# Performance work log

Measured on AMD Instinct MI355X. Metric: run time of the kernel, lower is better.

## Reference

```python
import jax, jax.numpy as jnp
import numpy as np

NR, NQ, NH, NV = 256, 64, 64, 4
B = 8192
NDRAW = 12
# zoneout probabilities from __init__ (applied deterministically, eval-mode expectation)
ZO_IJ, ZO_ID, ZO_GJ, ZO_GD = 0.3, 0.2, 0.3, 0.2


def _lin_init(key, fan_in, fan_out):
    kw, kb = jax.random.split(key)
    s = 1.0 / np.sqrt(fan_in)
    W = jax.random.uniform(kw, (fan_in, fan_out), jnp.float32, -s, s)
    b = jax.random.uniform(kb, (fan_out,), jnp.float32, -s, s)
    return W, b


def setup_inputs() -> dict:
    key = jax.random.key(0)
    ks = jax.random.split(key, 16)
    inp = {"ndraw": NDRAW}
    inp["cnd_repr"] = jax.random.normal(ks[0], (B, NR), jnp.float32)
    inp["qry_jrep"] = jax.random.normal(ks[1], (B, NQ), jnp.float32)
    inp["qry_drep"] = jax.random.normal(ks[2], (B, NQ), jnp.float32)
    inp["qry_v"] = jax.random.normal(ks[3], (B, NV), jnp.float32)
    for n in ["hi_j", "ci_j", "oi_j", "hi_d", "ci_d", "oi_d",
              "hg_j", "cg_j", "og_j", "hg_d", "cg_d", "og_d", "ug_j", "ug_d"]:
        inp[n] = jnp.zeros((B, NH), jnp.float32)
    # LSTM cells: W [in+nh, 4*nh]
    inp["W_ij"], inp["b_ij"] = _lin_init(ks[4], NR + NQ + NH + NH, 4 * NH)
    inp["W_id"], inp["b_id"] = _lin_init(ks[5], NR + NQ + NH + NH, 4 * NH)
    inp["W_gj"], inp["b_gj"] = _lin_init(ks[6], NR + NH + NH, 4 * NH)
    inp["W_gd"], inp["b_gd"] = _lin_init(ks[7], NR + NH + NV + NH, 4 * NH)
    # GaussianFactor heads: nh -> (mean, logv)
    inp["W_poj"], inp["b_poj"] = _lin_init(ks[8], NH, 2 * NH)
    inp["W_pod"], inp["b_pod"] = _lin_init(ks[9], NH, 2 * NH)
    inp["W_prj"], inp["b_prj"] = _lin_init(ks[10], NH, 2 * NH)
    inp["W_prd"], inp["b_prd"] = _lin_init(ks[11], NH, 2 * NH)
    # GeneratorDelta: cat(u, h) -> delta
    inp["W_dj"], inp["b_dj"] = _lin_init(ks[12], 2 * NH, NH)
    inp["W_dd"], inp["b_dd"] = _lin_init(ks[13], 2 * NH, NH)
    return inp


def _lstm(x, h, c, W, b, zo):
    g = jnp.concatenate([x, h], axis=1) @ W + b  # [B, 4*NH]
    i, f, gg, o = jnp.split(g, 4, axis=1)
    i, f, o = jax.nn.sigmoid(i), jax.nn.sigmoid(f), jax.nn.sigmoid(o)
    c_new = f * c + i * jnp.tanh(gg)
    h_new = o * jnp.tanh(c_new)
    # deterministic zoneout (expectation form)
    return zo * h + (1.0 - zo) * h_new, zo * c + (1.0 - zo) * c_new, o


def _gauss_stats(h, W, b):
    s = h @ W + b
    mean, logv = jnp.split(s, 2, axis=1)
    return mean, logv


def _delta(u, h, W, b):
    return jax.nn.leaky_relu(jnp.concatenate([u, h], axis=1) @ W + b)


def _forward(ndraw, cnd_repr, qry_jrep, qry_drep, qry_v,
             hi_j, ci_j, oi_j, hi_d, ci_d, oi_d,
             hg_j, cg_j, og_j, hg_d, cg_d, og_d, ug_j, ug_d,
             W_ij, b_ij, W_id, b_id, W_gj, b_gj, W_gd, b_gd,
             W_poj, b_poj, W_pod, b_pod, W_prj, b_prj, W_prd, b_prd,
             W_dj, b_dj, W_dd, b_dd):
    Bn = cnd_repr.shape[0]
    eps_j = jax.random.normal(jax.random.key(1), (ndraw, Bn, NH), jnp.float32)
    eps_d = jax.random.normal(jax.random.key(2), (ndraw, Bn, NH), jnp.float32)

    def step(carry, eps):
        (hi_j, ci_j, oi_j, hi_d, ci_d, oi_d,
         hg_j, cg_j, og_j, hg_d, cg_d, og_d, ug_j, ug_d) = carry
        ej, ed = eps
        # priors from current generator states (sampled z unused in loop)
        pr_m_j, pr_v_j = _gauss_stats(hg_j, W_prj, b_prj)
        pr_m_d, pr_v_d = _gauss_stats(hg_d, W_prd, b_prd)
        # inference states
        inp_ij = jnp.concatenate([cnd_repr, qry_jrep, hg_j], axis=1)
        inp_id = jnp.concatenate([cnd_repr, qry_drep, hg_d], axis=1)
        hi_j, ci_j, oi_j = _lstm(inp_ij, hi_j, ci_j, W_ij, b_ij, ZO_IJ)
        hi_d, ci_d, oi_d = _lstm(inp_id, hi_d, ci_d, W_id, b_id, ZO_ID)
        # posteriors + reparameterized samples
        po_m_j, po_v_j = _gauss_stats(hi_j, W_poj, b_poj)
        po_m_d, po_v_d = _gauss_stats(hi_d, W_pod, b_pod)
        z_j = po_m_j + jnp.exp(0.5 * po_v_j) * ej
        z_d = po_m_d + jnp.exp(0.5 * po_v_d) * ed
        # generator states
        inp_gj = jnp.concatenate([cnd_repr, z_j], axis=1)
        inp_gd = jnp.concatenate([cnd_repr, z_d, qry_v], axis=1)
        hg_j, cg_j, og_j = _lstm(inp_gj, hg_j, cg_j, W_gj, b_gj, ZO_GJ)
        hg_d, cg_d, og_d = _lstm(inp_gd, hg_d, cg_d, W_gd, b_gd, ZO_GD)
        # additive canvas updates
        ug_j = ug_j + _delta(ug_j, hg_j, W_dj, b_dj)
        ug_d = ug_d + _delta(ug_d, hg_d, W_dd, b_dd)
        carry = (hi_j, ci_j, oi_j, hi_d, ci_d, oi_d,
                 hg_j, cg_j, og_j, hg_d, cg_d, og_d, ug_j, ug_d)
        ys = (pr_m_j, pr_v_j, pr_m_d, pr_v_d, po_m_j, po_v_j, po_m_d, po_v_d)
        return carry, ys

    carry0 = (hi_j, ci_j, oi_j, hi_d, ci_d, oi_d,
              hg_j, cg_j, og_j, hg_d, cg_d, og_d, ug_j, ug_d)
    carry, ys = jax.lax.scan(step, carry0, (eps_j, eps_d))
    ug_j_out, ug_d_out = carry[-2], carry[-1]
    # pack: [2 + 8*ndraw, B, NH] (canvases then per-draw prior/posterior stats)
    out = jnp.concatenate([ug_j_out[None], ug_d_out[None]] + list(ys), axis=0)
    return out


def reference(ndraw, cnd_repr, qry_jrep, qry_drep, qry_v,
              hi_j, ci_j, oi_j, hi_d, ci_d, oi_d,
              hg_j, cg_j, og_j, hg_d, cg_d, og_d, ug_j, ug_d,
              W_ij, b_ij, W_id, b_id, W_gj, b_gj, W_gd, b_gd,
              W_poj, b_poj, W_pod, b_pod, W_prj, b_prj, W_prd, b_prd,
              W_dj, b_dj, W_dd, b_dd):
    return _forward(ndraw, cnd_repr, qry_jrep, qry_drep, qry_v,
                    hi_j, ci_j, oi_j, hi_d, ci_d, oi_d,
                    hg_j, cg_j, og_j, hg_d, cg_d, og_d, ug_j, ug_d,
                    W_ij, b_ij, W_id, b_id, W_gj, b_gj, W_gd, b_gd,
                    W_poj, b_poj, W_pod, b_pod, W_prj, b_prj, W_prd, b_prd,
                    W_dj, b_dj, W_dd, b_dd)
```

## Files before the change

kernel.cpp:

```cpp
#include <hip/hip_runtime.h>
#include <hip/hip_bf16.h>


typedef __attribute__((ext_vector_type(8))) short bf16x8;
typedef __attribute__((ext_vector_type(4))) float f32x4;

#define MFMA(A, Bv, C) __builtin_amdgcn_mfma_f32_16x16x32_bf16(A, Bv, C, 0, 0, 0)

#define FR_WI   0
#define FR_WG   32768
#define FR_WPR  65536
#define FR_WPO  73728
#define FR_WD   81920
#define FR_SIDE 90112

__device__ __forceinline__ unsigned short f2bf(float f) {
  unsigned u = __float_as_uint(f);
  return (unsigned short)((u + 0x7FFFu + ((u >> 16) & 1u)) >> 16);
}
__device__ __forceinline__ unsigned pk2(float a, float b) {
  return (unsigned)f2bf(a) | ((unsigned)f2bf(b) << 16);
}
__device__ __forceinline__ float sigf(float x) {
  return 1.0f / (1.0f + __expf(-x));
}
__device__ __forceinline__ float tanh_f(float x) {
  return 1.0f - 2.0f / (__expf(2.0f * x) + 1.0f);
}

__device__ __forceinline__ float eps_threefry(unsigned seed, unsigned idx) {
  unsigned x0 = 0u, x1 = idx;
  const unsigned ks0 = 0u, ks1 = seed, ks2 = seed ^ 0x1BD11BDAu;
  x0 += ks0; x1 += ks1;
#define TF_R(r) { x0 += x1; x1 = (x1 << (r)) | (x1 >> (32 - (r))); x1 ^= x0; }
  TF_R(13) TF_R(15) TF_R(26) TF_R(6)  x0 += ks1; x1 += ks2 + 1u;
  TF_R(17) TF_R(29) TF_R(16) TF_R(24) x0 += ks2; x1 += ks0 + 2u;
  TF_R(13) TF_R(15) TF_R(26) TF_R(6)  x0 += ks0; x1 += ks1 + 3u;
  TF_R(17) TF_R(29) TF_R(16) TF_R(24) x0 += ks1; x1 += ks2 + 4u;
  TF_R(13) TF_R(15) TF_R(26) TF_R(6)  x0 += ks2; x1 += ks0 + 5u;
#undef TF_R
  unsigned bits = x0 ^ x1;
  unsigned fb = (bits >> 9) | 0x3F800000u;
  const float lo = -0.99999994f;
  float f = __uint_as_float(fb) - 1.0f;
  float u = fmaxf(lo, f * 2.0f + lo);
  float w = -log1pf(-u * u);
  float p;
  if (w < 5.0f) {
    w -= 2.5f;
    p = 2.81022636e-08f;
    p = fmaf(p, w, 3.43273939e-07f);
    p = fmaf(p, w, -3.5233877e-06f);
    p = fmaf(p, w, -4.39150654e-06f);
    p = fmaf(p, w, 0.00021858087f);
    p = fmaf(p, w, -0.00125372503f);
    p = fmaf(p, w, -0.00417768164f);
    p = fmaf(p, w, 0.246640727f);
    p = fmaf(p, w, 1.50140941f);
  } else {
    w = sqrtf(w) - 3.0f;
    p = -0.000200214257f;
    p = fmaf(p, w, 0.000100950558f);
    p = fmaf(p, w, 0.00134934322f);
    p = fmaf(p, w, -0.00367342844f);
    p = fmaf(p, w, 0.00573950773f);
    p = fmaf(p, w, -0.0076224613f);
    p = fmaf(p, w, 0.00943887047f);
    p = fmaf(p, w, 1.00167406f);
    p = fmaf(p, w, 2.83297682f);
  }
  return 1.41421356f * (p * u);
}

__global__ __launch_bounds__(256) void GeRN_prepEps(
    const float* __restrict__ Wij, const float* __restrict__ Wid,
    const float* __restrict__ Wgj, const float* __restrict__ Wgd,
    const float* __restrict__ Wprj, const float* __restrict__ Wprd,
    const float* __restrict__ Wpoj, const float* __restrict__ Wpod,
    const float* __restrict__ Wdj, const float* __restrict__ Wdd,
    unsigned short* __restrict__ frB, unsigned short* __restrict__ sBs,
    float* __restrict__ ebuf, unsigned ndBN)
{
  if (blockIdx.x < 236) {
    const int vb = blockIdx.x * 4 + (threadIdx.x >> 6);
    const int l = threadIdx.x & 63;
    if (vb < 352) {
      const int s = vb / 176;
      int tt = vb % 176;
      const float* W; int ldw, rb, NT, kt, nt; size_t doff;
      if (tt < 64)       { W = s ? Wid : Wij; ldw = 256; NT = 16; kt = tt >> 4; nt = tt & 15;
                           rb = 320 + kt * 32; doff = FR_WI; }
      else if (tt < 128) { tt -= 64; W = s ? Wgd : Wgj; ldw = 256; NT = 16; kt = tt >> 4; nt = tt & 15;
                           rb = (kt < 2) ? 256 + kt * 32 : (s ? 324 : 320) + (kt - 2) * 32; doff = FR_WG; }
      else if (tt < 144) { tt -= 128; W = s ? Wprd : Wprj; ldw = 128; NT = 8; kt = tt >> 3; nt = tt & 7;
                           rb = kt * 32; doff = FR_WPR; }
      else if (tt < 160) { tt -= 144; W = s ? Wpod : Wpoj; ldw = 128; NT = 8; kt = tt >> 3; nt = tt & 7;
                           rb = kt * 32; doff = FR_WPO; }
      else               { tt -= 160; W = s ? Wdd : Wdj; ldw = 64; NT = 4; kt = tt >> 2; nt = tt & 3;
                           rb = (kt < 2) ? kt * 32 : 64 + (kt - 2) * 32; doff = FR_WD; }
      unsigned short* dst = frB + (size_t)s * FR_SIDE + doff
                          + ((size_t)(kt * NT + nt) * 64 + l) * 8;
      const int kk = (l >> 4) * 8;
      const int c = nt * 16 + (l & 15);
      #pragma unroll
      for (int j = 0; j < 8; ++j)
        dst[j] = f2bf(W[(size_t)(rb + kk + j) * ldw + c]);
    } else {
      int bb = vb - 352;
      int mat, base;
      if (bb < 160)      { mat = 0; base = 0; }
      else if (bb < 320) { mat = 1; base = 160; }
      else if (bb < 448) { mat = 2; base = 320; }
      else               { mat = 3; base = 448; }
      int tt = bb - base;
      int kk = tt >> 4, nt = tt & 15;
      const float* W = mat == 0 ? Wij : mat == 1 ? Wid : mat == 2 ? Wgj : Wgd;
      const int c = nt * 16 + (l & 15);
      const int kl0 = (l >> 4) * 8;
      unsigned short* dst = sBs + ((size_t)bb * 64 + l) * 8;
      if (mat == 3 && kk == 8) {
        #pragma unroll
        for (int j = 0; j < 8; ++j) {
          int klo = kl0 + j;
          dst[j] = (klo < 4) ? f2bf(W[(size_t)(320 + klo) * 256 + c]) : (unsigned short)0;
        }
      } else {
        int rb = (kk < 8) ? kk * 32 : 256 + (kk - 8) * 32;
        #pragma unroll
        for (int j = 0; j < 8; ++j)
          dst[j] = f2bf(W[(size_t)(rb + kl0 + j) * 256 + c]);
      }
    }
  } else {
    unsigned j0 = ((blockIdx.x - 236) * 256u + threadIdx.x) * 8u;
    const unsigned total = 2u * ndBN;
    if (j0 >= total) return;
    const unsigned s = (j0 >= ndBN) ? 1u : 0u;
    const unsigned i0 = j0 - s * ndBN;
    const unsigned seed = 1u + s;
    float v[8];
    #pragma unroll
    for (int k = 0; k < 8; ++k) v[k] = eps_threefry(seed, i0 + (unsigned)k);
    float4 a = {v[0], v[1], v[2], v[3]};
    float4 b = {v[4], v[5], v[6], v[7]};
    *(float4*)(ebuf + j0) = a;
    *(float4*)(ebuf + j0 + 4) = b;
  }
}

#define WR_FR(buf, row, c, v) \
  fr[buf][(c) >> 5][((row) & 15) + (((c) >> 3) & 3) * 16][(c) & 7] = f2bf(v)
#define LD_FR(buf, kt) (*(const bf16x8*)&fr[buf][kt][l][0])
#define LD_B(off, kt, nt, NT) \
  (*(const bf16x8*)(FB + (off) + (((kt) * (NT) + (nt)) * 64 + l) * 8))
#define LD_S(idx) (*(const bf16x8*)&sBs[((size_t)(idx) * 64 + l) * 8])
#define LD_H(ph, kt, nt) \
  (*(const bf16x8*)&shH[(ph) * 8192 + (((kt) * 8 + (nt)) * 64 + l) * 8])

template<int USE_EPS>
__global__ __launch_bounds__(256, 2) void GeRN_recur(
    const unsigned short* __restrict__ frB,
    const unsigned short* __restrict__ sBs,
    const float* __restrict__ cnd, const float* __restrict__ qjg,
    const float* __restrict__ qdg, const float* __restrict__ qvg,
    const float* __restrict__ bij, const float* __restrict__ bid,
    const float* __restrict__ bgj, const float* __restrict__ bgd,
    const float* __restrict__ bprj, const float* __restrict__ bprd,
    const float* __restrict__ bpoj, const float* __restrict__ bpod,
    const float* __restrict__ bdj,  const float* __restrict__ bdd,
    const float* __restrict__ hi_j0, const float* __restrict__ ci_j0,
    const float* __restrict__ hi_d0, const float* __restrict__ ci_d0,
    const float* __restrict__ hg_j0, const float* __restrict__ cg_j0,
    const float* __restrict__ hg_d0, const float* __restrict__ cg_d0,
    const float* __restrict__ ug_j0, const float* __restrict__ ug_d0,
    const float* __restrict__ eps_buf, unsigned ndBN,
    float* __restrict__ out, int B, int nd)
{
  alignas(16) __shared__ unsigned short fr[6][2][64][8];
  alignas(16) __shared__ unsigned short shH[16384];
  alignas(16) __shared__ unsigned short As[11][64][8];

  const int tid = threadIdx.x;
  const int l   = tid & 63;
  const int wv  = tid >> 6;
  const int s   = blockIdx.x & 1;
  const int rbk = blockIdx.x >> 1;
  const int r0  = (l >> 4) * 4;
  const int col = wv * 16 + (l & 15);
  const int bbase = rbk * 16;
  const size_t BN = (size_t)B * 64;

  const float* hi0 = s ? hi_d0 : hi_j0;  const float* ci0 = s ? ci_d0 : ci_j0;
  const float* hg0 = s ? hg_d0 : hg_j0;  const float* cg0 = s ? cg_d0 : cg_j0;
  const float* ug0 = s ? ug_d0 : ug_j0;
  const float* BPR = s ? bprd : bprj;
  const float* BPO = s ? bpod : bpoj;
  const float* BD  = s ? bdd  : bdj;
  const float* BI  = s ? bid  : bij;
  const float* BG  = s ? bgd  : bgj;
  const float* qq  = s ? qdg  : qjg;
  const unsigned short* FB = frB + (size_t)s * FR_SIDE;

  bf16x8 wi[4][4], wg[4][4], wd[4];
  #pragma unroll
  for (int kt = 0; kt < 4; ++kt) {
    #pragma unroll
    for (int g = 0; g < 4; ++g) {
      wi[kt][g] = LD_B(FR_WI, kt, g * 4 + wv, 16);
      wg[kt][g] = LD_B(FR_WG, kt, g * 4 + wv, 16);
    }
    wd[kt] = LD_B(FR_WD, kt, wv, 4);
  }
  #pragma unroll
  for (int kt = 0; kt < 4; ++kt) {
    #pragma unroll
    for (int g = 0; g < 4; ++g)
      asm volatile("" : "+v"(wi[kt][g]), "+v"(wg[kt][g]));
    asm volatile("" : "+v"(wd[kt]));
  }

  {
    const float4* src = (const float4*)(FB + FR_WPR);
    float4* dst = (float4*)shH;
    for (int i = tid; i < 2048; i += 256) dst[i] = src[i];
  }
  for (int i = tid; i < 16 * 44; i += 256) {
    int r = i / 44, kc = i % 44;
    float v[8];
    if (kc < 32) {
      const float4* p = (const float4*)&cnd[(size_t)(bbase + r) * 256 + kc * 8];
      float4 x0 = p[0], x1 = p[1];
      v[0] = x0.x; v[1] = x0.y; v[2] = x0.z; v[3] = x0.w;
      v[4] = x1.x; v[5] = x1.y; v[6] = x1.z; v[7] = x1.w;
    } else if (kc < 40) {
      const float4* p = (const float4*)&qq[(size_t)(bbase + r) * 64 + (kc - 32) * 8];
      float4 x0 = p[0], x1 = p[1];
      v[0] = x0.x; v[1] = x0.y; v[2] = x0.z; v[3] = x0.w;
      v[4] = x1.x; v[5] = x1.y; v[6] = x1.z; v[7] = x1.w;
    } else if (kc == 40 && s) {
      #pragma unroll
      for (int j = 0; j < 8; ++j) v[j] = (j < 4) ? qvg[(size_t)(bbase + r) * 4 + j] : 0.0f;
    } else {
      #pragma unroll
      for (int j = 0; j < 8; ++j) v[j] = 0.0f;
    }
    int kt = kc >> 2;
    int lane = r + (kc & 3) * 16;
    uint4 wq;
    wq.x = pk2(v[0], v[1]); wq.y = pk2(v[2], v[3]);
    wq.z = pk2(v[4], v[5]); wq.w = pk2(v[6], v[7]);
    *(uint4*)&As[kt][lane][0] = wq;
  }
  __syncthreads();

  f32x4 preI[4], preG[4];
  {
    const int ktB_I = s ? 160 : 0;
    const int ktB_G = s ? 448 : 320;
    const int ktN_G = s ? 9 : 8;
    #pragma unroll
    for (int g = 0; g < 4; ++g) {
      float bi = BI[g * 64 + col];
      float bg = BG[g * 64 + col];
      f32x4 vi = {bi, bi, bi, bi};
      f32x4 vg = {bg, bg, bg, bg};
      preI[g] = vi; preG[g] = vg;
    }
    #pragma unroll
    for (int kk = 0; kk < 10; ++kk) {
      bf16x8 a = *(const bf16x8*)&As[kk][l][0];
      #pragma unroll
      for (int g = 0; g < 4; ++g)
        preI[g] = MFMA(a, LD_S(ktB_I + kk * 16 + g * 4 + wv), preI[g]);
    }
    for (int kk = 0; kk < ktN_G; ++kk) {
      int ktA = (kk < 8) ? kk : 10;
      bf16x8 a = *(const bf16x8*)&As[ktA][l][0];
      #pragma unroll
      for (int g = 0; g < 4; ++g)
        preG[g] = MFMA(a, LD_S(ktB_G + kk * 16 + g * 4 + wv), preG[g]);
    }
  }

  float hi_[4], ci_[4], hg_[4], cg_[4], u_[4];
  #pragma unroll
  for (int r = 0; r < 4; ++r) {
    size_t gi = (size_t)(bbase + r0 + r) * 64 + col;
    hi_[r] = hi0[gi]; ci_[r] = ci0[gi];
    hg_[r] = hg0[gi]; cg_[r] = cg0[gi];
    u_[r]  = ug0[gi];
  }
  const float bprm = BPR[col], bprv = BPR[64 + col];
  const float bpom = BPO[col], bpov = BPO[64 + col];
  const float bd   = BD[col];

  #pragma unroll
  for (int r = 0; r < 4; ++r) {
    WR_FR(0, r0 + r, col, hi_[r]);
    WR_FR(2, r0 + r, col, hg_[r]);
    WR_FR(4, r0 + r, col, u_[r]);
  }
  __syncthreads();

  const float zo = s ? 0.2f : 0.3f, zo1 = 1.0f - zo;

  const unsigned gi0 = (unsigned)((bbase + r0) * 64 + col);
  float* o_prm = out + (size_t)(2 + (2 * s) * nd) * BN + gi0;
  float* o_prv = out + (size_t)(2 + (2 * s + 1) * nd) * BN + gi0;
  float* o_pom = out + (size_t)(2 + (4 + 2 * s) * nd) * BN + gi0;
  float* o_pov = out + (size_t)(2 + (5 + 2 * s) * nd) * BN + gi0;
  unsigned e0 = gi0;
  const unsigned BNu = (unsigned)BN;
  const unsigned eseed = 1u + (unsigned)s;
  const float* ep = USE_EPS ? (eps_buf + (size_t)s * ndBN + gi0) : (const float*)0;

  for (int t = 0; t < nd; ++t) {
    const int cb = t & 1;
    float epre[4];
    if (USE_EPS) {
      #pragma unroll
      for (int r = 0; r < 4; ++r) epre[r] = ep[r * 64];
    }
    bf16x8 a_hg0 = LD_FR(2, 0), a_hg1 = LD_FR(2, 1);
    bf16x8 a_hi0 = LD_FR(cb, 0), a_hi1 = LD_FR(cb, 1);

    {
      f32x4 am = {bprm, bprm, bprm, bprm};
      f32x4 av = {bprv, bprv, bprv, bprv};
      am = MFMA(a_hg0, LD_H(0, 0, wv), am);
      am = MFMA(a_hg1, LD_H(0, 1, wv), am);
      av = MFMA(a_hg0, LD_H(0, 0, wv + 4), av);
      av = MFMA(a_hg1, LD_H(0, 1, wv + 4), av);
      #pragma unroll
      for (int r = 0; r < 4; ++r) {
        o_prm[r * 64] = am[r];
        o_prv[r * 64] = av[r];
      }
    }
    {
      f32x4 acc[4];
      #pragma unroll
      for (int g = 0; g < 4; ++g) acc[g] = preI[g];
      #pragma unroll
      for (int g = 0; g < 4; ++g) {
        acc[g] = MFMA(a_hg0, wi[0][g], acc[g]);
        acc[g] = MFMA(a_hg1, wi[1][g], acc[g]);
        acc[g] = MFMA(a_hi0, wi[2][g], acc[g]);
        acc[g] = MFMA(a_hi1, wi[3][g], acc[g]);
      }
      #pragma unroll
      for (int r = 0; r < 4; ++r) {
        float ig = sigf(acc[0][r]), fg = sigf(acc[1][r]);
        float gg = tanh_f(acc[2][r]), og = sigf(acc[3][r]);
        float cn = fmaf(fg, ci_[r], ig * gg);
        float hn = og * tanh_f(cn);
        hi_[r] = fmaf(zo, hi_[r], zo1 * hn);
        ci_[r] = fmaf(zo, ci_[r], zo1 * cn);
        WR_FR(cb ^ 1, r0 + r, col, hi_[r]);
      }
    }
    __syncthreads();

    {
      bf16x8 a0 = LD_FR(cb ^ 1, 0), a1 = LD_FR(cb ^ 1, 1);
      f32x4 am = {bpom, bpom, bpom, bpom};
      f32x4 av = {bpov, bpov, bpov, bpov};
      am = MFMA(a0, LD_H(1, 0, wv), am);
      am = MFMA(a1, LD_H(1, 1, wv), am);
      av = MFMA(a0, LD_H(1, 0, wv + 4), av);
      av = MFMA(a1, LD_H(1, 1, wv + 4), av);
      #pragma unroll
      for (int r = 0; r < 4; ++r) {
        o_pom[r * 64] = am[r];
        o_pov[r * 64] = av[r];
        float e = USE_EPS ? epre[r] : eps_threefry(eseed, e0 + r * 64);
        float z = fmaf(__expf(0.5f * av[r]), e, am[r]);
        WR_FR(3, r0 + r, col, z);
      }
    }
    __syncthreads();

    {
      bf16x8 az0 = LD_FR(3, 0), az1 = LD_FR(3, 1);
      f32x4 acc[4];
      #pragma unroll
      for (int g = 0; g < 4; ++g) acc[g] = preG[g];
      #pragma unroll
      for (int g = 0; g < 4; ++g) {
        acc[g] = MFMA(az0,   wg[0][g], acc[g]);
        acc[g] = MFMA(az1,   wg[1][g], acc[g]);
        acc[g] = MFMA(a_hg0, wg[2][g], acc[g]);
        acc[g] = MFMA(a_hg1, wg[3][g], acc[g]);
      }
      #pragma unroll
      for (int r = 0; r < 4; ++r) {
        float ig = sigf(acc[0][r]), fg = sigf(acc[1][r]);
        float gg = tanh_f(acc[2][r]), og = sigf(acc[3][r]);
        float cn = fmaf(fg, cg_[r], ig * gg);
        float hn = og * tanh_f(cn);
        hg_[r] = fmaf(zo, hg_[r], zo1 * hn);
        cg_[r] = fmaf(zo, cg_[r], zo1 * cn);
        WR_FR(2, r0 + r, col, hg_[r]);
      }
    }
    __syncthreads();

    {
      bf16x8 au0 = LD_FR(4 + cb, 0), au1 = LD_FR(4 + cb, 1);
      bf16x8 ah0 = LD_FR(2, 0), ah1 = LD_FR(2, 1);
      f32x4 acc = {bd, bd, bd, bd};
      acc = MFMA(au0, wd[0], acc);
      acc = MFMA(au1, wd[1], acc);
      acc = MFMA(ah0, wd[2], acc);
      acc = MFMA(ah1, wd[3], acc);
      #pragma unroll
      for (int r = 0; r < 4; ++r) {
        float a = acc[r];
        float d = a > 0.0f ? a : 0.01f * a;
        u_[r] += d;
        WR_FR(4 + (cb ^ 1), r0 + r, col, u_[r]);
      }
    }
    __syncthreads();

    o_prm += BN; o_prv += BN; o_pom += BN; o_pov += BN;
    e0 += BNu;
    if (USE_EPS) ep += BN;
  }

  #pragma unroll
  for (int r = 0; r < 4; ++r) {
    size_t gi = (size_t)(bbase + r0 + r) * 64 + col;
    out[(size_t)s * BN + gi] = u_[r];
  }
}

extern "C" void kernel_launch(void* const* d_in, const int* in_sizes, int n_in,
                              void* d_out, int out_size, void* d_ws, size_t ws_size,
                              hipStream_t stream)
{
  const float* cnd = (const float*)d_in[1];
  const float* qj  = (const float*)d_in[2];
  const float* qd  = (const float*)d_in[3];
  const float* qv  = (const float*)d_in[4];
  const float* hi_j0 = (const float*)d_in[5];
  const float* ci_j0 = (const float*)d_in[6];
  const float* hi_d0 = (const float*)d_in[8];
  const float* ci_d0 = (const float*)d_in[9];
  const float* hg_j0 = (const float*)d_in[11];
  const float* cg_j0 = (const float*)d_in[12];
  const float* hg_d0 = (const float*)d_in[14];
  const float* cg_d0 = (const float*)d_in[15];
  const float* ug_j0 = (const float*)d_in[17];
  const float* ug_d0 = (const float*)d_in[18];
  const float* Wij = (const float*)d_in[19]; const float* bij = (const float*)d_in[20];
  const float* Wid = (const float*)d_in[21]; const float* bid = (const float*)d_in[22];
  const float* Wgj = (const float*)d_in[23]; const float* bgj = (const float*)d_in[24];
  const float* Wgd = (const float*)d_in[25]; const float* bgd = (const float*)d_in[26];
  const float* Wpoj = (const float*)d_in[27]; const float* bpoj = (const float*)d_in[28];
  const float* Wpod = (const float*)d_in[29]; const float* bpod = (const float*)d_in[30];
  const float* Wprj = (const float*)d_in[31]; const float* bprj = (const float*)d_in[32];
  const float* Wprd = (const float*)d_in[33]; const float* bprd = (const float*)d_in[34];
  const float* Wdj = (const float*)d_in[35]; const float* bdj = (const float*)d_in[36];
  const float* Wdd = (const float*)d_in[37]; const float* bdd = (const float*)d_in[38];

  const int B = in_sizes[1] / 256;
  const int slots = out_size / (B * 64);
  const int nd = (slots - 2) / 8;

  unsigned short* frB = (unsigned short*)d_ws;
  unsigned short* sBs = frB + 2 * FR_SIDE;
  size_t epsOff = (size_t)2 * FR_SIDE * 2 + (size_t)592 * 512 * 2;
  epsOff = (epsOff + 255) & ~(size_t)255;
  const unsigned ndBN = (unsigned)((size_t)nd * B * 64);
  float* epsBuf = (float*)((char*)d_ws + epsOff);
  const bool useEps = ws_size >= epsOff + (size_t)2 * ndBN * 4;
  float* out = (float*)d_out;

  const int epsBlocks = useEps ? (int)((2u * ndBN + 2047u) / 2048u) : 0;
  GeRN_prepEps<<<236 + epsBlocks, 256, 0, stream>>>(
      Wij, Wid, Wgj, Wgd, Wprj, Wprd, Wpoj, Wpod, Wdj, Wdd, frB, sBs,
      epsBuf, ndBN);
  if (useEps) {
    GeRN_recur<1><<<2 * (B / 16), 256, 0, stream>>>(
        frB, sBs, cnd, qj, qd, qv, bij, bid, bgj, bgd,
        bprj, bprd, bpoj, bpod, bdj, bdd,
        hi_j0, ci_j0, hi_d0, ci_d0, hg_j0, cg_j0, hg_d0, cg_d0, ug_j0, ug_d0,
        epsBuf, ndBN, out, B, nd);
  } else {
    GeRN_recur<0><<<2 * (B / 16), 256, 0, stream>>>(
        frB, sBs, cnd, qj, qd, qv, bij, bid, bgj, bgd,
        bprj, bprd, bpoj, bpod, bdj, bdd,
        hi_j0, ci_j0, hi_d0, ci_d0, hg_j0, cg_j0, hg_d0, cg_d0, ug_j0, ug_d0,
        (const float*)0, ndBN, out, B, nd);
  }
}
```

Baseline: 204.6 us.

## Stream recurrent weights from global memory instead of registers and LDS

After: 478.1 us. 2.34x slower.

```diff
diff --git a/kernel.cpp b/kernel.cpp
--- a/kernel.cpp
+++ b/kernel.cpp
@@ -154,11 +154,9 @@
 #define LD_B(off, kt, nt, NT) \
   (*(const bf16x8*)(FB + (off) + (((kt) * (NT) + (nt)) * 64 + l) * 8))
 #define LD_S(idx) (*(const bf16x8*)&sBs[((size_t)(idx) * 64 + l) * 8])
-#define LD_H(ph, kt, nt) \
-  (*(const bf16x8*)&shH[(ph) * 8192 + (((kt) * 8 + (nt)) * 64 + l) * 8])
 
 template<int USE_EPS>
-__global__ __launch_bounds__(256, 2) void GeRN_recur(
+__global__ __launch_bounds__(256, 4) void GeRN_recur(
     const unsigned short* __restrict__ frB,
     const unsigned short* __restrict__ sBs,
     const float* __restrict__ cnd, const float* __restrict__ qjg,
@@ -177,7 +175,6 @@
     float* __restrict__ out, int B, int nd)
 {
   alignas(16) __shared__ unsigned short fr[6][2][64][8];
-  alignas(16) __shared__ unsigned short shH[16384];
   alignas(16) __shared__ unsigned short As[11][64][8];
 
   const int tid = threadIdx.x;
@@ -201,29 +198,6 @@
   const float* qq  = s ? qdg  : qjg;
   const unsigned short* FB = frB + (size_t)s * FR_SIDE;
 
-  bf16x8 wi[4][4], wg[4][4], wd[4];
-  #pragma unroll
-  for (int kt = 0; kt < 4; ++kt) {
-    #pragma unroll
-    for (int g = 0; g < 4; ++g) {
-      wi[kt][g] = LD_B(FR_WI, kt, g * 4 + wv, 16);
-      wg[kt][g] = LD_B(FR_WG, kt, g * 4 + wv, 16);
-    }
-    wd[kt] = LD_B(FR_WD, kt, wv, 4);
-  }
-  #pragma unroll
-  for (int kt = 0; kt < 4; ++kt) {
-    #pragma unroll
-    for (int g = 0; g < 4; ++g)
-      asm volatile("" : "+v"(wi[kt][g]), "+v"(wg[kt][g]));
-    asm volatile("" : "+v"(wd[kt]));
-  }
-
-  {
-    const float4* src = (const float4*)(FB + FR_WPR);
-    float4* dst = (float4*)shH;
-    for (int i = tid; i < 2048; i += 256) dst[i] = src[i];
-  }
   for (int i = tid; i < 16 * 44; i += 256) {
     int r = i / 44, kc = i % 44;
     float v[8];
@@ -327,10 +301,10 @@
     {
       f32x4 am = {bprm, bprm, bprm, bprm};
       f32x4 av = {bprv, bprv, bprv, bprv};
-      am = MFMA(a_hg0, LD_H(0, 0, wv), am);
-      am = MFMA(a_hg1, LD_H(0, 1, wv), am);
-      av = MFMA(a_hg0, LD_H(0, 0, wv + 4), av);
-      av = MFMA(a_hg1, LD_H(0, 1, wv + 4), av);
+      am = MFMA(a_hg0, LD_B(FR_WPR, 0, wv, 8), am);
+      am = MFMA(a_hg1, LD_B(FR_WPR, 1, wv, 8), am);
+      av = MFMA(a_hg0, LD_B(FR_WPR, 0, wv + 4, 8), av);
+      av = MFMA(a_hg1, LD_B(FR_WPR, 1, wv + 4, 8), av);
       #pragma unroll
       for (int r = 0; r < 4; ++r) {
         o_prm[r * 64] = am[r];
@@ -343,10 +317,10 @@
       for (int g = 0; g < 4; ++g) acc[g] = preI[g];
       #pragma unroll
       for (int g = 0; g < 4; ++g) {
-        acc[g] = MFMA(a_hg0, wi[0][g], acc[g]);
-        acc[g] = MFMA(a_hg1, wi[1][g], acc[g]);
-        acc[g] = MFMA(a_hi0, wi[2][g], acc[g]);
-        acc[g] = MFMA(a_hi1, wi[3][g], acc[g]);
+        acc[g] = MFMA(a_hg0, LD_B(FR_WI, 0, g * 4 + wv, 16), acc[g]);
+        acc[g] = MFMA(a_hg1, LD_B(FR_WI, 1, g * 4 + wv, 16), acc[g]);
+        acc[g] = MFMA(a_hi0, LD_B(FR_WI, 2, g * 4 + wv, 16), acc[g]);
+        acc[g] = MFMA(a_hi1, LD_B(FR_WI, 3, g * 4 + wv, 16), acc[g]);
       }
       #pragma unroll
       for (int r = 0; r < 4; ++r) {
@@ -365,10 +339,10 @@
       bf16x8 a0 = LD_FR(cb ^ 1, 0), a1 = LD_FR(cb ^ 1, 1);
       f32x4 am = {bpom, bpom, bpom, bpom};
       f32x4 av = {bpov, bpov, bpov, bpov};
-      am = MFMA(a0, LD_H(1, 0, wv), am);
-      am = MFMA(a1, LD_H(1, 1, wv), am);
-      av = MFMA(a0, LD_H(1, 0, wv + 4), av);
-      av = MFMA(a1, LD_H(1, 1, wv + 4), av);
+      am = MFMA(a0, LD_B(FR_WPO, 0, wv, 8), am);
+      am = MFMA(a1, LD_B(FR_WPO, 1, wv, 8), am);
+      av = MFMA(a0, LD_B(FR_WPO, 0, wv + 4, 8), av);
+      av = MFMA(a1, LD_B(FR_WPO, 1, wv + 4, 8), av);
       #pragma unroll
       for (int r = 0; r < 4; ++r) {
         o_pom[r * 64] = am[r];
@@ -387,10 +361,10 @@
       for (int g = 0; g < 4; ++g) acc[g] = preG[g];
       #pragma unroll
       for (int g = 0; g < 4; ++g) {
-        acc[g] = MFMA(az0,   wg[0][g], acc[g]);
-        acc[g] = MFMA(az1,   wg[1][g], acc[g]);
-        acc[g] = MFMA(a_hg0, wg[2][g], acc[g]);
-        acc[g] = MFMA(a_hg1, wg[3][g], acc[g]);
+        acc[g] = MFMA(az0,   LD_B(FR_WG, 0, g * 4 + wv, 16), acc[g]);
+        acc[g] = MFMA(az1,   LD_B(FR_WG, 1, g * 4 + wv, 16), acc[g]);
+        acc[g] = MFMA(a_hg0, LD_B(FR_WG, 2, g * 4 + wv, 16), acc[g]);
+        acc[g] = MFMA(a_hg1, LD_B(FR_WG, 3, g * 4 + wv, 16), acc[g]);
       }
       #pragma unroll
       for (int r = 0; r < 4; ++r) {
@@ -409,10 +383,10 @@
       bf16x8 au0 = LD_FR(4 + cb, 0), au1 = LD_FR(4 + cb, 1);
       bf16x8 ah0 = LD_FR(2, 0), ah1 = LD_FR(2, 1);
       f32x4 acc = {bd, bd, bd, bd};
-      acc = MFMA(au0, wd[0], acc);
-      acc = MFMA(au1, wd[1], acc);
-      acc = MFMA(ah0, wd[2], acc);
-      acc = MFMA(ah1, wd[3], acc);
+      acc = MFMA(au0, LD_B(FR_WD, 0, wv, 4), acc);
+      acc = MFMA(au1, LD_B(FR_WD, 1, wv, 4), acc);
+      acc = MFMA(ah0, LD_B(FR_WD, 2, wv, 4), acc);
+      acc = MFMA(ah1, LD_B(FR_WD, 3, wv, 4), acc);
       #pragma unroll
       for (int r = 0; r < 4; ++r) {
         float a = acc[r];
```
